# Kernel optimization log

Measured on AMD Instinct MI355X. Metric: run time of the kernel, lower is better.

Reference implementation:

```python
import jax, jax.numpy as jnp
import numpy as np

WS = 8            # window size -> N = 64 tokens per window
DIM = 256
HEADS = 8
BWIN = 4096       # B * num_windows (512x512 image, batch 1)


def _rel_pos_index(ws):
    # exact replica of the torch buffer construction
    coords = np.stack(np.meshgrid(np.arange(ws), np.arange(ws), indexing='ij'))  # (2, ws, ws)
    cf = coords.reshape(2, -1)
    rel = cf[:, :, None] - cf[:, None, :]          # (2, N, N)
    rel = rel.transpose(1, 2, 0).astype(np.int64)  # (N, N, 2)
    rel[..., 0] += ws - 1
    rel[..., 1] += ws - 1
    rel[..., 0] *= 2 * ws - 1
    return np.clip(rel.sum(-1), -1000, 1000)       # (N, N)


def setup_inputs() -> dict:
    key = jax.random.key(0)
    ks = jax.random.split(key, 6)
    N = WS * WS
    x = jax.random.normal(ks[0], (BWIN, N, DIM), dtype=jnp.float32)
    var = jax.random.normal(ks[1], (BWIN, N, DIM), dtype=jnp.float32)
    W_qkv = jax.random.normal(ks[2], (DIM, 3 * DIM), dtype=jnp.float32) * 0.02
    b_qkv = jnp.zeros((3 * DIM,), dtype=jnp.float32)
    W_proj = jax.random.normal(ks[3], (DIM, DIM), dtype=jnp.float32) * 0.02
    b_proj = jnp.zeros((DIM,), dtype=jnp.float32)
    bias_table = jax.random.normal(ks[4], ((2 * WS - 1) * (2 * WS - 1), HEADS), dtype=jnp.float32) * 0.02
    rel_index = jnp.asarray(_rel_pos_index(WS), dtype=jnp.int32)
    return {"x": x, "var": var, "W_qkv": W_qkv, "b_qkv": b_qkv,
            "W_proj": W_proj, "b_proj": b_proj,
            "bias_table": bias_table, "rel_index": rel_index}


def reference(x, var, W_qkv, b_qkv, W_proj, b_proj, bias_table, rel_index):
    B_, N, C = x.shape
    H = HEADS
    hd = C // H
    scale = hd ** -0.5
    topk = int(0.8 * N)  # int(0.8 * ws * ws) = 51

    # --- topk variance modulation mask ---
    var_self = jnp.einsum('bnd,bmd->bnm', var, var)              # (B_, N, N)
    idx = jax.lax.top_k(var_self, topk)[1]                       # (B_, N, topk)
    b_ix = jnp.arange(B_)[:, None, None]
    n_ix = jnp.arange(N)[None, :, None]
    mask = jnp.zeros((B_, N, N), x.dtype).at[b_ix, n_ix, idx].set(1.0)
    mod = jnp.where(mask > 0, jnp.asarray(1.0, x.dtype), jnp.asarray(1.2, x.dtype))
    mod = mod[:, None]                                           # (B_, 1, N, N)

    # --- windowed self-attention with modulation + relative position bias ---
    qkv = (x @ W_qkv + b_qkv).reshape(B_, N, 3, H, hd).transpose(2, 0, 3, 1, 4)
    q, k, v = qkv[0], qkv[1], qkv[2]                             # each (B_, H, N, hd)
    dots = jnp.einsum('bhnd,bhmd->bhnm', q * scale, k) * mod     # (B_, H, N, N)
    bias = bias_table[rel_index.reshape(-1)].reshape(N, N, H).transpose(2, 0, 1)
    dots = dots + bias[None]
    attn = jax.nn.softmax(dots, axis=-1)
    out = jnp.einsum('bhnm,bhmd->bhnd', attn, v)                 # (B_, H, N, hd)
    out = out.transpose(0, 2, 1, 3).reshape(B_, N, C)
    return out @ W_proj + b_proj
```

## Files before the change

### kernel.cpp

```cpp
#include <hip/hip_runtime.h>

#define NTOK 64
#define DIM 256
#define NH 8
#define HD 32
#define BWIN 4096
#define TOPK 51

typedef _Float16 f16;
typedef _Float16 f16x8 __attribute__((ext_vector_type(8)));
typedef _Float16 f16x4 __attribute__((ext_vector_type(4)));
typedef float f32x4 __attribute__((ext_vector_type(4)));

#define MFMA(a, b, c) __builtin_amdgcn_mfma_f32_16x16x32_f16((a), (b), (c), 0, 0, 0)

__global__ void prep_kernel(const float* __restrict__ Wqkv, const float* __restrict__ Wproj,
                            const float* __restrict__ bias_table, const int* __restrict__ rel_index,
                            f16* __restrict__ Wqt, f16* __restrict__ Wpt, float* __restrict__ biasp) {
    int tid = blockIdx.x * blockDim.x + threadIdx.x;
    const int nq = 768 * 256, np = 256 * 256, nb = NH * NTOK * NTOK;
    for (int i = tid; i < nq + np + nb; i += gridDim.x * blockDim.x) {
        if (i < nq) {
            int o = i >> 8, d = i & 255;
            Wqt[i] = (f16)Wqkv[d * 768 + o];
        } else if (i < nq + np) {
            int j = i - nq;
            int o = j >> 8, d = j & 255;
            Wpt[j] = (f16)Wproj[d * 256 + o];
        } else {
            int j = i - nq - np;
            int h = j >> 12;
            int nm = j & 4095;
            biasp[j] = bias_table[rel_index[nm] * NH + h];
        }
    }
}

__global__ __launch_bounds__(256, 2)
void swin_kernel(const float* __restrict__ x, const float* __restrict__ var,
                 const float* __restrict__ b_qkv, const float* __restrict__ b_proj,
                 const f16* __restrict__ Wqt, const f16* __restrict__ Wpt,
                 const float* __restrict__ biasp, float* __restrict__ out) {
    __shared__ __align__(16) union {
        struct {
            f16 xv[64][264];
            union {
                float vs[64][65];
                f16 p[64][72];
            } s2;
            unsigned char mod[64][64];
            f16 qm[64][40];
            f16 km[64][40];
            f16 vT[32][72];
            f16 oh[64][40];
        } a;
        struct {
            f16 pad[64 * 264];
            f16 lo[64][264];
        } b;
    } sm;

    const int tid = threadIdx.x;
    const int lane = tid & 63;
    const int w = tid >> 6;
    const int lc = lane & 15;
    const int lq = lane >> 4;
    const int bwin = blockIdx.x;

    const float* varp = var + (size_t)bwin * NTOK * DIM;
    const float* xp = x + (size_t)bwin * NTOK * DIM;
    float* outp = out + (size_t)bwin * NTOK * DIM;

    #pragma unroll
    for (int it = 0; it < 16; ++it) {
        int i = it * 256 + tid;
        int r = i >> 6, c4 = i & 63;
        float4 v4 = ((const float4*)varp)[i];
        f16 h0 = (f16)v4.x, h1 = (f16)v4.y, h2 = (f16)v4.z, h3 = (f16)v4.w;
        f16x4 hv = {h0, h1, h2, h3};
        f16x4 lv = {(f16)(v4.x - (float)h0), (f16)(v4.y - (float)h1),
                    (f16)(v4.z - (float)h2), (f16)(v4.w - (float)h3)};
        *(f16x4*)&sm.a.xv[r][c4 * 4] = hv;
        *(f16x4*)&sm.b.lo[r][c4 * 4] = lv;
    }
    __syncthreads();

    f32x4 vacc[4];
    #pragma unroll
    for (int mt = 0; mt < 4; ++mt) vacc[mt] = (f32x4){0.f, 0.f, 0.f, 0.f};
    #pragma unroll
    for (int ks = 0; ks < 8; ++ks) {
        int k0 = ks * 32 + lq * 8;
        f16x8 ahi = *(const f16x8*)&sm.a.xv[w * 16 + lc][k0];
        f16x8 alo = *(const f16x8*)&sm.b.lo[w * 16 + lc][k0];
        #pragma unroll
        for (int mt = 0; mt < 4; ++mt) {
            f16x8 bhi = *(const f16x8*)&sm.a.xv[mt * 16 + lc][k0];
            f16x8 blo = *(const f16x8*)&sm.b.lo[mt * 16 + lc][k0];
            vacc[mt] = MFMA(ahi, bhi, vacc[mt]);
            vacc[mt] = MFMA(ahi, blo, vacc[mt]);
            vacc[mt] = MFMA(alo, bhi, vacc[mt]);
        }
    }
    __syncthreads();
    #pragma unroll
    for (int mt = 0; mt < 4; ++mt)
        #pragma unroll
        for (int r = 0; r < 4; ++r)
            sm.a.s2.vs[w * 16 + lq * 4 + r][mt * 16 + lc] = vacc[mt][r];
    __syncthreads();

    float4 xl[16];
    #pragma unroll
    for (int it = 0; it < 16; ++it) xl[it] = ((const float4*)xp)[it * 256 + tid];

    {
        int n = tid >> 2, part = tid & 3;
        float vm[16];
        int cnt[16];
        #pragma unroll
        for (int i = 0; i < 16; ++i) { vm[i] = sm.a.s2.vs[n][part * 16 + i]; cnt[i] = 0; }
        for (int j = 0; j < 64; ++j) {
            float vj = sm.a.s2.vs[n][j];
            #pragma unroll
            for (int i = 0; i < 16; ++i) {
                int mi = part * 16 + i;
                cnt[i] += (int)((vj > vm[i]) | ((vj == vm[i]) & (j < mi)));
            }
        }
        #pragma unroll
        for (int i = 0; i < 16; ++i)
            sm.a.mod[n][part * 16 + i] = (cnt[i] < TOPK) ? 1 : 0;
    }

    #pragma unroll
    for (int it = 0; it < 16; ++it) {
        int i = it * 256 + tid;
        int r = i >> 6, c4 = i & 63;
        float4 v4 = xl[it];
        f16x4 hv = {(f16)v4.x, (f16)v4.y, (f16)v4.z, (f16)v4.w};
        *(f16x4*)&sm.a.xv[r][c4 * 4] = hv;
    }
    __syncthreads();

    f32x4 facc[4][4];
    #pragma unroll
    for (int rt = 0; rt < 4; ++rt)
        #pragma unroll
        for (int pt = 0; pt < 4; ++pt) facc[rt][pt] = (f32x4){0.f, 0.f, 0.f, 0.f};

    const float scale = 0.17677669529663687f;

    for (int h = 0; h < NH; ++h) {
        f32x4 qa[2], ka[2], va[2];
        #pragma unroll
        for (int ct = 0; ct < 2; ++ct) {
            qa[ct] = (f32x4){0.f, 0.f, 0.f, 0.f};
            ka[ct] = (f32x4){0.f, 0.f, 0.f, 0.f};
            va[ct] = (f32x4){0.f, 0.f, 0.f, 0.f};
        }
        #pragma unroll
        for (int ks = 0; ks < 8; ++ks) {
            int k0 = ks * 32 + lq * 8;
            f16x8 af = *(const f16x8*)&sm.a.xv[w * 16 + lc][k0];
            #pragma unroll
            for (int ct = 0; ct < 2; ++ct) {
                int oq = h * 32 + ct * 16 + lc;
                f16x8 bq = *(const f16x8*)&Wqt[(size_t)oq * 256 + k0];
                f16x8 bk = *(const f16x8*)&Wqt[(size_t)(256 + oq) * 256 + k0];
                f16x8 bv = *(const f16x8*)&Wqt[(size_t)(512 + oq) * 256 + k0];
                qa[ct] = MFMA(af, bq, qa[ct]);
                ka[ct] = MFMA(af, bk, ka[ct]);
                va[ct] = MFMA(af, bv, va[ct]);
            }
        }
        #pragma unroll
        for (int ct = 0; ct < 2; ++ct) {
            int oq = h * 32 + ct * 16 + lc;
            float bq = b_qkv[oq], bk = b_qkv[256 + oq], bv = b_qkv[512 + oq];
            #pragma unroll
            for (int r = 0; r < 4; ++r) {
                int row = w * 16 + lq * 4 + r;
                sm.a.qm[row][ct * 16 + lc] = (f16)(qa[ct][r] + bq);
                sm.a.km[row][ct * 16 + lc] = (f16)(ka[ct][r] + bk);
                sm.a.vT[ct * 16 + lc][row] = (f16)(va[ct][r] + bv);
            }
        }
        __syncthreads();

        f32x4 dacc[4];
        {
            f16x8 qf = *(const f16x8*)&sm.a.qm[w * 16 + lc][lq * 8];
            #pragma unroll
            for (int mt = 0; mt < 4; ++mt) {
                f16x8 kf = *(const f16x8*)&sm.a.km[mt * 16 + lc][lq * 8];
                f32x4 zz = {0.f, 0.f, 0.f, 0.f};
                dacc[mt] = MFMA(qf, kf, zz);
            }
        }
        float pv[4][4], mx[4], lsum[4];
        #pragma unroll
        for (int r = 0; r < 4; ++r) mx[r] = -1e30f;
        #pragma unroll
        for (int mt = 0; mt < 4; ++mt)
            #pragma unroll
            for (int r = 0; r < 4; ++r) {
                int row = w * 16 + lq * 4 + r;
                int col = mt * 16 + lc;
                float modv = sm.a.mod[row][col] ? 1.0f : 1.2f;
                float bv = biasp[(h * 64 + row) * 64 + col];
                float t = dacc[mt][r] * scale * modv + bv;
                pv[mt][r] = t;
                mx[r] = fmaxf(mx[r], t);
            }
        #pragma unroll
        for (int r = 0; r < 4; ++r) {
            float m = mx[r];
            m = fmaxf(m, __shfl_xor(m, 1));
            m = fmaxf(m, __shfl_xor(m, 2));
            m = fmaxf(m, __shfl_xor(m, 4));
            m = fmaxf(m, __shfl_xor(m, 8));
            mx[r] = m;
            lsum[r] = 0.f;
        }
        #pragma unroll
        for (int mt = 0; mt < 4; ++mt)
            #pragma unroll
            for (int r = 0; r < 4; ++r) {
                float e = __expf(pv[mt][r] - mx[r]);
                pv[mt][r] = e;
                lsum[r] += e;
            }
        #pragma unroll
        for (int r = 0; r < 4; ++r) {
            float s = lsum[r];
            s += __shfl_xor(s, 1);
            s += __shfl_xor(s, 2);
            s += __shfl_xor(s, 4);
            s += __shfl_xor(s, 8);
            lsum[r] = s;
        }
        #pragma unroll
        for (int mt = 0; mt < 4; ++mt)
            #pragma unroll
            for (int r = 0; r < 4; ++r)
                sm.a.s2.p[w * 16 + lq * 4 + r][mt * 16 + lc] = (f16)pv[mt][r];
        __syncthreads();

        f32x4 oacc[2];
        #pragma unroll
        for (int ct = 0; ct < 2; ++ct) oacc[ct] = (f32x4){0.f, 0.f, 0.f, 0.f};
        #pragma unroll
        for (int ks = 0; ks < 2; ++ks) {
            f16x8 pf = *(const f16x8*)&sm.a.s2.p[w * 16 + lc][ks * 32 + lq * 8];
            #pragma unroll
            for (int ct = 0; ct < 2; ++ct) {
                f16x8 vf = *(const f16x8*)&sm.a.vT[ct * 16 + lc][ks * 32 + lq * 8];
                oacc[ct] = MFMA(pf, vf, oacc[ct]);
            }
        }
        float rl[4];
        #pragma unroll
        for (int r = 0; r < 4; ++r) rl[r] = 1.0f / lsum[r];
        #pragma unroll
        for (int ct = 0; ct < 2; ++ct)
            #pragma unroll
            for (int r = 0; r < 4; ++r)
                sm.a.oh[w * 16 + lq * 4 + r][ct * 16 + lc] = (f16)(oacc[ct][r] * rl[r]);
        __syncthreads();

        #pragma unroll
        for (int rt = 0; rt < 4; ++rt) {
            f16x8 af = *(const f16x8*)&sm.a.oh[rt * 16 + lc][lq * 8];
            #pragma unroll
            for (int pt = 0; pt < 4; ++pt) {
                f16x8 bf = *(const f16x8*)&Wpt[(size_t)(w * 64 + pt * 16 + lc) * 256 + h * 32 + lq * 8];
                facc[rt][pt] = MFMA(af, bf, facc[rt][pt]);
            }
        }
        __syncthreads();
    }

    #pragma unroll
    for (int pt = 0; pt < 4; ++pt) {
        int col = w * 64 + pt * 16 + lc;
        float bp = b_proj[col];
        #pragma unroll
        for (int rt = 0; rt < 4; ++rt)
            #pragma unroll
            for (int r = 0; r < 4; ++r) {
                int row = rt * 16 + lq * 4 + r;
                outp[row * 256 + col] = facc[rt][pt][r] + bp;
            }
    }
}

extern "C" void kernel_launch(void* const* d_in, const int* in_sizes, int n_in,
                              void* d_out, int out_size, void* d_ws, size_t ws_size,
                              hipStream_t stream) {
    const float* x          = (const float*)d_in[0];
    const float* var        = (const float*)d_in[1];
    const float* W_qkv      = (const float*)d_in[2];
    const float* b_qkv      = (const float*)d_in[3];
    const float* W_proj     = (const float*)d_in[4];
    const float* b_proj     = (const float*)d_in[5];
    const float* bias_table = (const float*)d_in[6];
    const int*   rel_index  = (const int*)d_in[7];

    f16*   Wqt   = (f16*)d_ws;
    f16*   Wpt   = (f16*)((char*)d_ws + 393216);
    float* biasp = (float*)((char*)d_ws + 524288);

    prep_kernel<<<288, 256, 0, stream>>>(W_qkv, W_proj, bias_table, rel_index, Wqt, Wpt, biasp);
    swin_kernel<<<BWIN, 256, 0, stream>>>(x, var, b_qkv, b_proj, Wqt, Wpt, biasp, (float*)d_out);
}
```

Measured before the change: 1.418 ms.

## Assign one wave per head with register-resident Q/K/V and 512-thread blocks

Restructures the attention kernel so each of 8 waves owns one head. The waves compute Q, K and V for that head with MFMA and keep them in registers. Scores are computed transposed with 16x16x16 MFMA so the accumulator layout feeds the P·V product directly, which removes the per-head shared-memory round trips and most __syncthreads. The bias table is pre-transposed, the mask is stored transposed, and the projection combines all heads' outputs from shared memory at the end. The trade-offs are more registers per thread and a launch bound of 512 threads with min 4 blocks, which may cause spills or limit occupancy.

```diff
diff --git a/kernel.cpp b/kernel.cpp
--- a/kernel.cpp
+++ b/kernel.cpp
@@ -3,7 +3,6 @@
 #define NTOK 64
 #define DIM 256
 #define NH 8
-#define HD 32
 #define BWIN 4096
 #define TOPK 51
 
@@ -12,7 +11,8 @@
 typedef _Float16 f16x4 __attribute__((ext_vector_type(4)));
 typedef float f32x4 __attribute__((ext_vector_type(4)));
 
-#define MFMA(a, b, c) __builtin_amdgcn_mfma_f32_16x16x32_f16((a), (b), (c), 0, 0, 0)
+#define MFMA32(a, b, c) __builtin_amdgcn_mfma_f32_16x16x32_f16((a), (b), (c), 0, 0, 0)
+#define MFMA16(a, b, c) __builtin_amdgcn_mfma_f32_16x16x16f16((a), (b), (c), 0, 0, 0)
 
 __global__ void prep_kernel(const float* __restrict__ Wqkv, const float* __restrict__ Wproj,
                             const float* __restrict__ bias_table, const int* __restrict__ rel_index,
@@ -31,33 +31,25 @@
             int j = i - nq - np;
             int h = j >> 12;
             int nm = j & 4095;
-            biasp[j] = bias_table[rel_index[nm] * NH + h];
+            int n = nm >> 6, m = nm & 63;
+            biasp[(h << 12) + (m << 6) + n] = bias_table[rel_index[nm] * NH + h];
         }
     }
 }
 
-__global__ __launch_bounds__(256, 2)
+__global__ __launch_bounds__(512, 4)
 void swin_kernel(const float* __restrict__ x, const float* __restrict__ var,
                  const float* __restrict__ b_qkv, const float* __restrict__ b_proj,
                  const f16* __restrict__ Wqt, const f16* __restrict__ Wpt,
                  const float* __restrict__ biasp, float* __restrict__ out) {
-    __shared__ __align__(16) union {
-        struct {
-            f16 xv[64][264];
-            union {
-                float vs[64][65];
-                f16 p[64][72];
-            } s2;
-            unsigned char mod[64][64];
-            f16 qm[64][40];
-            f16 km[64][40];
-            f16 vT[32][72];
-            f16 oh[64][40];
-        } a;
-        struct {
-            f16 pad[64 * 264];
+    __shared__ __align__(16) struct {
+        f16 xv[64][264];
+        union {
+            f16 oh[NH][64][40];
             f16 lo[64][264];
-        } b;
+            float vs[64][65];
+        } u;
+        unsigned char modT[64][65];
     } sm;
 
     const int tid = threadIdx.x;
@@ -71,227 +63,284 @@
     const float* xp = x + (size_t)bwin * NTOK * DIM;
     float* outp = out + (size_t)bwin * NTOK * DIM;
 
-    #pragma unroll
-    for (int it = 0; it < 16; ++it) {
-        int i = it * 256 + tid;
+    float4 v4[8], x4[8];
+    #pragma unroll
+    for (int it = 0; it < 8; ++it) v4[it] = ((const float4*)varp)[it * 512 + tid];
+    #pragma unroll
+    for (int it = 0; it < 8; ++it) x4[it] = ((const float4*)xp)[it * 512 + tid];
+    #pragma unroll
+    for (int it = 0; it < 8; ++it) {
+        int i = it * 512 + tid;
         int r = i >> 6, c4 = i & 63;
-        float4 v4 = ((const float4*)varp)[i];
-        f16 h0 = (f16)v4.x, h1 = (f16)v4.y, h2 = (f16)v4.z, h3 = (f16)v4.w;
+        float4 vv = v4[it];
+        f16 h0 = (f16)vv.x, h1 = (f16)vv.y, h2 = (f16)vv.z, h3 = (f16)vv.w;
         f16x4 hv = {h0, h1, h2, h3};
-        f16x4 lv = {(f16)(v4.x - (float)h0), (f16)(v4.y - (float)h1),
-                    (f16)(v4.z - (float)h2), (f16)(v4.w - (float)h3)};
-        *(f16x4*)&sm.a.xv[r][c4 * 4] = hv;
-        *(f16x4*)&sm.b.lo[r][c4 * 4] = lv;
+        f16x4 lv = {(f16)(vv.x - (float)h0), (f16)(vv.y - (float)h1),
+                    (f16)(vv.z - (float)h2), (f16)(vv.w - (float)h3)};
+        *(f16x4*)&sm.xv[r][c4 * 4] = hv;
+        *(f16x4*)&sm.u.lo[r][c4 * 4] = lv;
     }
     __syncthreads();
 
-    f32x4 vacc[4];
-    #pragma unroll
-    for (int mt = 0; mt < 4; ++mt) vacc[mt] = (f32x4){0.f, 0.f, 0.f, 0.f};
-    #pragma unroll
-    for (int ks = 0; ks < 8; ++ks) {
-        int k0 = ks * 32 + lq * 8;
-        f16x8 ahi = *(const f16x8*)&sm.a.xv[w * 16 + lc][k0];
-        f16x8 alo = *(const f16x8*)&sm.b.lo[w * 16 + lc][k0];
-        #pragma unroll
-        for (int mt = 0; mt < 4; ++mt) {
-            f16x8 bhi = *(const f16x8*)&sm.a.xv[mt * 16 + lc][k0];
-            f16x8 blo = *(const f16x8*)&sm.b.lo[mt * 16 + lc][k0];
-            vacc[mt] = MFMA(ahi, bhi, vacc[mt]);
-            vacc[mt] = MFMA(ahi, blo, vacc[mt]);
-            vacc[mt] = MFMA(alo, bhi, vacc[mt]);
-        }
-    }
-    __syncthreads();
-    #pragma unroll
-    for (int mt = 0; mt < 4; ++mt)
-        #pragma unroll
-        for (int r = 0; r < 4; ++r)
-            sm.a.s2.vs[w * 16 + lq * 4 + r][mt * 16 + lc] = vacc[mt][r];
-    __syncthreads();
-
-    float4 xl[16];
-    #pragma unroll
-    for (int it = 0; it < 16; ++it) xl[it] = ((const float4*)xp)[it * 256 + tid];
-
-    {
-        int n = tid >> 2, part = tid & 3;
-        float vm[16];
-        int cnt[16];
-        #pragma unroll
-        for (int i = 0; i < 16; ++i) { vm[i] = sm.a.s2.vs[n][part * 16 + i]; cnt[i] = 0; }
-        for (int j = 0; j < 64; ++j) {
-            float vj = sm.a.s2.vs[n][j];
-            #pragma unroll
-            for (int i = 0; i < 16; ++i) {
-                int mi = part * 16 + i;
-                cnt[i] += (int)((vj > vm[i]) | ((vj == vm[i]) & (j < mi)));
-            }
-        }
-        #pragma unroll
-        for (int i = 0; i < 16; ++i)
-            sm.a.mod[n][part * 16 + i] = (cnt[i] < TOPK) ? 1 : 0;
-    }
-
-    #pragma unroll
-    for (int it = 0; it < 16; ++it) {
-        int i = it * 256 + tid;
-        int r = i >> 6, c4 = i & 63;
-        float4 v4 = xl[it];
-        f16x4 hv = {(f16)v4.x, (f16)v4.y, (f16)v4.z, (f16)v4.w};
-        *(f16x4*)&sm.a.xv[r][c4 * 4] = hv;
-    }
-    __syncthreads();
-
-    f32x4 facc[4][4];
-    #pragma unroll
-    for (int rt = 0; rt < 4; ++rt)
-        #pragma unroll
-        for (int pt = 0; pt < 4; ++pt) facc[rt][pt] = (f32x4){0.f, 0.f, 0.f, 0.f};
-
-    const float scale = 0.17677669529663687f;
-
-    for (int h = 0; h < NH; ++h) {
-        f32x4 qa[2], ka[2], va[2];
-        #pragma unroll
-        for (int ct = 0; ct < 2; ++ct) {
-            qa[ct] = (f32x4){0.f, 0.f, 0.f, 0.f};
-            ka[ct] = (f32x4){0.f, 0.f, 0.f, 0.f};
-            va[ct] = (f32x4){0.f, 0.f, 0.f, 0.f};
-        }
+    {
+        const int rs = w >> 1;
+        f32x4 vacc[2];
+        vacc[0] = (f32x4){0.f, 0.f, 0.f, 0.f};
+        vacc[1] = (f32x4){0.f, 0.f, 0.f, 0.f};
         #pragma unroll
         for (int ks = 0; ks < 8; ++ks) {
             int k0 = ks * 32 + lq * 8;
-            f16x8 af = *(const f16x8*)&sm.a.xv[w * 16 + lc][k0];
-            #pragma unroll
-            for (int ct = 0; ct < 2; ++ct) {
-                int oq = h * 32 + ct * 16 + lc;
-                f16x8 bq = *(const f16x8*)&Wqt[(size_t)oq * 256 + k0];
-                f16x8 bk = *(const f16x8*)&Wqt[(size_t)(256 + oq) * 256 + k0];
-                f16x8 bv = *(const f16x8*)&Wqt[(size_t)(512 + oq) * 256 + k0];
-                qa[ct] = MFMA(af, bq, qa[ct]);
-                ka[ct] = MFMA(af, bk, ka[ct]);
-                va[ct] = MFMA(af, bv, va[ct]);
-            }
+            f16x8 ahi = *(const f16x8*)&sm.xv[rs * 16 + lc][k0];
+            f16x8 alo = *(const f16x8*)&sm.u.lo[rs * 16 + lc][k0];
+            #pragma unroll
+            for (int m = 0; m < 2; ++m) {
+                int mt = (w & 1) * 2 + m;
+                f16x8 bhi = *(const f16x8*)&sm.xv[mt * 16 + lc][k0];
+                f16x8 blo = *(const f16x8*)&sm.u.lo[mt * 16 + lc][k0];
+                vacc[m] = MFMA32(ahi, bhi, vacc[m]);
+                vacc[m] = MFMA32(ahi, blo, vacc[m]);
+                vacc[m] = MFMA32(alo, bhi, vacc[m]);
+            }
+        }
+        __syncthreads();
+        #pragma unroll
+        for (int m = 0; m < 2; ++m) {
+            int mt = (w & 1) * 2 + m;
+            #pragma unroll
+            for (int r = 0; r < 4; ++r)
+                sm.u.vs[rs * 16 + lq * 4 + r][mt * 16 + lc] = vacc[m][r];
+        }
+    }
+    #pragma unroll
+    for (int it = 0; it < 8; ++it) {
+        int i = it * 512 + tid;
+        int r = i >> 6, c4 = i & 63;
+        float4 vv = x4[it];
+        f16x4 hv = {(f16)vv.x, (f16)vv.y, (f16)vv.z, (f16)vv.w};
+        *(f16x4*)&sm.xv[r][c4 * 4] = hv;
+    }
+    __syncthreads();
+
+    {
+        int n = tid >> 3, part = tid & 7;
+        float vm[8];
+        int cnt[8];
+        #pragma unroll
+        for (int i = 0; i < 8; ++i) { vm[i] = sm.u.vs[n][part * 8 + i]; cnt[i] = 0; }
+        for (int j = 0; j < 64; ++j) {
+            float vj = sm.u.vs[n][j];
+            #pragma unroll
+            for (int i = 0; i < 8; ++i) {
+                int mi = part * 8 + i;
+                cnt[i] += (int)((vj > vm[i]) | ((vj == vm[i]) & (j < mi)));
+            }
+        }
+        #pragma unroll
+        for (int i = 0; i < 8; ++i)
+            sm.modT[part * 8 + i][n] = (cnt[i] < TOPK) ? 1 : 0;
+    }
+    __syncthreads();
+
+    const int h = w;
+    const float scale = 0.17677669529663687f;
+    const f16* Wq = Wqt + (size_t)(h * 32) * 256;
+    const f16* Wk = Wqt + (size_t)(256 + h * 32) * 256;
+    const f16* Wv = Wqt + (size_t)(512 + h * 32) * 256;
+
+    float bqr[2][4], bkr[2][4], bvl[2];
+    #pragma unroll
+    for (int ot = 0; ot < 2; ++ot)
+        #pragma unroll
+        for (int r = 0; r < 4; ++r) {
+            bqr[ot][r] = b_qkv[h * 32 + ot * 16 + lq * 4 + r];
+            bkr[ot][r] = b_qkv[256 + h * 32 + ot * 16 + lq * 4 + r];
+        }
+    #pragma unroll
+    for (int cd = 0; cd < 2; ++cd) bvl[cd] = b_qkv[512 + h * 32 + cd * 16 + lc];
+
+    f16x4 qop[2][4], kop[2][4], vop[2][4];
+    {
+        f32x4 acc[2][4];
+        #pragma unroll
+        for (int a = 0; a < 2; ++a)
+            #pragma unroll
+            for (int b = 0; b < 4; ++b) acc[a][b] = (f32x4){0.f, 0.f, 0.f, 0.f};
+        #pragma unroll
+        for (int ks = 0; ks < 8; ++ks) {
+            int k0 = ks * 32 + lq * 8;
+            f16x8 xf[4], wf[2];
+            #pragma unroll
+            for (int tt = 0; tt < 4; ++tt) xf[tt] = *(const f16x8*)&sm.xv[tt * 16 + lc][k0];
+            #pragma unroll
+            for (int ot = 0; ot < 2; ++ot) wf[ot] = *(const f16x8*)&Wq[(size_t)(ot * 16 + lc) * 256 + k0];
+            #pragma unroll
+            for (int ot = 0; ot < 2; ++ot)
+                #pragma unroll
+                for (int tt = 0; tt < 4; ++tt)
+                    acc[ot][tt] = MFMA32(wf[ot], xf[tt], acc[ot][tt]);
+        }
+        #pragma unroll
+        for (int ot = 0; ot < 2; ++ot)
+            #pragma unroll
+            for (int tt = 0; tt < 4; ++tt)
+                #pragma unroll
+                for (int r = 0; r < 4; ++r)
+                    qop[ot][tt][r] = (f16)((acc[ot][tt][r] + bqr[ot][r]) * scale);
+        #pragma unroll
+        for (int a = 0; a < 2; ++a)
+            #pragma unroll
+            for (int b = 0; b < 4; ++b) acc[a][b] = (f32x4){0.f, 0.f, 0.f, 0.f};
+        #pragma unroll
+        for (int ks = 0; ks < 8; ++ks) {
+            int k0 = ks * 32 + lq * 8;
+            f16x8 xf[4], wf[2];
+            #pragma unroll
+            for (int tt = 0; tt < 4; ++tt) xf[tt] = *(const f16x8*)&sm.xv[tt * 16 + lc][k0];
+            #pragma unroll
+            for (int ot = 0; ot < 2; ++ot) wf[ot] = *(const f16x8*)&Wk[(size_t)(ot * 16 + lc) * 256 + k0];
+            #pragma unroll
+            for (int ot = 0; ot < 2; ++ot)
+                #pragma unroll
+                for (int tt = 0; tt < 4; ++tt)
+                    acc[ot][tt] = MFMA32(wf[ot], xf[tt], acc[ot][tt]);
+        }
+        #pragma unroll
+        for (int ot = 0; ot < 2; ++ot)
+            #pragma unroll
+            for (int tt = 0; tt < 4; ++tt)
+                #pragma unroll
+                for (int r = 0; r < 4; ++r)
+                    kop[ot][tt][r] = (f16)(acc[ot][tt][r] + bkr[ot][r]);
+        #pragma unroll
+        for (int a = 0; a < 2; ++a)
+            #pragma unroll
+            for (int b = 0; b < 4; ++b) acc[a][b] = (f32x4){0.f, 0.f, 0.f, 0.f};
+        #pragma unroll
+        for (int ks = 0; ks < 8; ++ks) {
+            int k0 = ks * 32 + lq * 8;
+            f16x8 xf[4], wf[2];
+            #pragma unroll
+            for (int tt = 0; tt < 4; ++tt) xf[tt] = *(const f16x8*)&sm.xv[tt * 16 + lc][k0];
+            #pragma unroll
+            for (int cd = 0; cd < 2; ++cd) wf[cd] = *(const f16x8*)&Wv[(size_t)(cd * 16 + lc) * 256 + k0];
+            #pragma unroll
+            for (int cd = 0; cd < 2; ++cd)
+                #pragma unroll
+                for (int tt = 0; tt < 4; ++tt)
+                    acc[cd][tt] = MFMA32(xf[tt], wf[cd], acc[cd][tt]);
+        }
+        #pragma unroll
+        for (int cd = 0; cd < 2; ++cd)
+            #pragma unroll
+            for (int tt = 0; tt < 4; ++tt)
+                #pragma unroll
+                for (int r = 0; r < 4; ++r)
+                    vop[cd][tt][r] = (f16)(acc[cd][tt][r] + bvl[cd]);
+    }
+
+    f16x4 pop[4][4];
+    float ls[4];
+    const float* bt = biasp + h * 4096;
+    #pragma unroll
+    for (int ci = 0; ci < 4; ++ci) {
+        f32x4 st[4];
+        #pragma unroll
+        for (int rj = 0; rj < 4; ++rj) {
+            f32x4 z = (f32x4){0.f, 0.f, 0.f, 0.f};
+            z = MFMA16(kop[0][rj], qop[0][ci], z);
+            st[rj] = MFMA16(kop[1][rj], qop[1][ci], z);
+        }
+        float mx = -1e30f;
+        #pragma unroll
+        for (int rj = 0; rj < 4; ++rj)
+            #pragma unroll
+            for (int r = 0; r < 4; ++r) {
+                int j = rj * 16 + lq * 4 + r;
+                float modv = sm.modT[j][ci * 16 + lc] ? 1.0f : 1.2f;
+                float t = st[rj][r] * modv + bt[j * 64 + ci * 16 + lc];
+                st[rj][r] = t;
+                mx = fmaxf(mx, t);
+            }
+        mx = fmaxf(mx, __shfl_xor(mx, 16));
+        mx = fmaxf(mx, __shfl_xor(mx, 32));
+        float s = 0.f;
+        #pragma unroll
+        for (int rj = 0; rj < 4; ++rj)
+            #pragma unroll
+            for (int r = 0; r < 4; ++r) {
+                float e = __expf(st[rj][r] - mx);
+                st[rj][r] = e;
+                s += e;
+            }
+        s += __shfl_xor(s, 16);
+        s += __shfl_xor(s, 32);
+        ls[ci] = s;
+        #pragma unroll
+        for (int rj = 0; rj < 4; ++rj)
+            #pragma unroll
+            for (int r = 0; r < 4; ++r)
+                pop[ci][rj][r] = (f16)st[rj][r];
+    }
+
+    {
+        f32x4 oacc[4][2];
+        #pragma unroll
+        for (int ti = 0; ti < 4; ++ti)
+            #pragma unroll
+            for (int cd = 0; cd < 2; ++cd) oacc[ti][cd] = (f32x4){0.f, 0.f, 0.f, 0.f};
+        #pragma unroll
+        for (int kc = 0; kc < 4; ++kc)
+            #pragma unroll
+            for (int ti = 0; ti < 4; ++ti)
+                #pragma unroll
+                for (int cd = 0; cd < 2; ++cd)
+                    oacc[ti][cd] = MFMA16(pop[ti][kc], vop[cd][kc], oacc[ti][cd]);
+        float inv[4];
+        #pragma unroll
+        for (int ci = 0; ci < 4; ++ci) inv[ci] = 1.0f / ls[ci];
+        #pragma unroll
+        for (int ti = 0; ti < 4; ++ti)
+            #pragma unroll
+            for (int r = 0; r < 4; ++r) {
+                float rl = __shfl(inv[ti], lq * 4 + r);
+                #pragma unroll
+                for (int cd = 0; cd < 2; ++cd)
+                    sm.u.oh[w][ti * 16 + lq * 4 + r][cd * 16 + lc] = (f16)(oacc[ti][cd][r] * rl);
+            }
+    }
+    __syncthreads();
+
+    {
+        f32x4 facc[4][2];
+        #pragma unroll
+        for (int rt = 0; rt < 4; ++rt)
+            #pragma unroll
+            for (int ct = 0; ct < 2; ++ct) facc[rt][ct] = (f32x4){0.f, 0.f, 0.f, 0.f};
+        #pragma unroll
+        for (int hh = 0; hh < NH; ++hh) {
+            f16x8 pf[4], wfp[2];
+            #pragma unroll
+            for (int rt = 0; rt < 4; ++rt)
+                pf[rt] = *(const f16x8*)&sm.u.oh[hh][rt * 16 + lc][lq * 8];
+            #pragma unroll
+            for (int ct = 0; ct < 2; ++ct)
+                wfp[ct] = *(const f16x8*)&Wpt[(size_t)(w * 32 + ct * 16 + lc) * 256 + hh * 32 + lq * 8];
+            #pragma unroll
+            for (int rt = 0; rt < 4; ++rt)
+                #pragma unroll
+                for (int ct = 0; ct < 2; ++ct)
+                    facc[rt][ct] = MFMA32(pf[rt], wfp[ct], facc[rt][ct]);
         }
         #pragma unroll
         for (int ct = 0; ct < 2; ++ct) {
-            int oq = h * 32 + ct * 16 + lc;
-            float bq = b_qkv[oq], bk = b_qkv[256 + oq], bv = b_qkv[512 + oq];
-            #pragma unroll
-            for (int r = 0; r < 4; ++r) {
-                int row = w * 16 + lq * 4 + r;
-                sm.a.qm[row][ct * 16 + lc] = (f16)(qa[ct][r] + bq);
-                sm.a.km[row][ct * 16 + lc] = (f16)(ka[ct][r] + bk);
-                sm.a.vT[ct * 16 + lc][row] = (f16)(va[ct][r] + bv);
-            }
-        }
-        __syncthreads();
-
-        f32x4 dacc[4];
-        {
-            f16x8 qf = *(const f16x8*)&sm.a.qm[w * 16 + lc][lq * 8];
-            #pragma unroll
-            for (int mt = 0; mt < 4; ++mt) {
-                f16x8 kf = *(const f16x8*)&sm.a.km[mt * 16 + lc][lq * 8];
-                f32x4 zz = {0.f, 0.f, 0.f, 0.f};
-                dacc[mt] = MFMA(qf, kf, zz);
-            }
-        }
-        float pv[4][4], mx[4], lsum[4];
-        #pragma unroll
-        for (int r = 0; r < 4; ++r) mx[r] = -1e30f;
-        #pragma unroll
-        for (int mt = 0; mt < 4; ++mt)
-            #pragma unroll
-            for (int r = 0; r < 4; ++r) {
-                int row = w * 16 + lq * 4 + r;
-                int col = mt * 16 + lc;
-                float modv = sm.a.mod[row][col] ? 1.0f : 1.2f;
-                float bv = biasp[(h * 64 + row) * 64 + col];
-                float t = dacc[mt][r] * scale * modv + bv;
-                pv[mt][r] = t;
-                mx[r] = fmaxf(mx[r], t);
-            }
-        #pragma unroll
-        for (int r = 0; r < 4; ++r) {
-            float m = mx[r];
-            m = fmaxf(m, __shfl_xor(m, 1));
-            m = fmaxf(m, __shfl_xor(m, 2));
-            m = fmaxf(m, __shfl_xor(m, 4));
-            m = fmaxf(m, __shfl_xor(m, 8));
-            mx[r] = m;
-            lsum[r] = 0.f;
-        }
-        #pragma unroll
-        for (int mt = 0; mt < 4; ++mt)
-            #pragma unroll
-            for (int r = 0; r < 4; ++r) {
-                float e = __expf(pv[mt][r] - mx[r]);
-                pv[mt][r] = e;
-                lsum[r] += e;
-            }
-        #pragma unroll
-        for (int r = 0; r < 4; ++r) {
-            float s = lsum[r];
-            s += __shfl_xor(s, 1);
-            s += __shfl_xor(s, 2);
-            s += __shfl_xor(s, 4);
-            s += __shfl_xor(s, 8);
-            lsum[r] = s;
-        }
-        #pragma unroll
-        for (int mt = 0; mt < 4; ++mt)
-            #pragma unroll
-            for (int r = 0; r < 4; ++r)
-                sm.a.s2.p[w * 16 + lq * 4 + r][mt * 16 + lc] = (f16)pv[mt][r];
-        __syncthreads();
-
-        f32x4 oacc[2];
-        #pragma unroll
-        for (int ct = 0; ct < 2; ++ct) oacc[ct] = (f32x4){0.f, 0.f, 0.f, 0.f};
-        #pragma unroll
-        for (int ks = 0; ks < 2; ++ks) {
-            f16x8 pf = *(const f16x8*)&sm.a.s2.p[w * 16 + lc][ks * 32 + lq * 8];
-            #pragma unroll
-            for (int ct = 0; ct < 2; ++ct) {
-                f16x8 vf = *(const f16x8*)&sm.a.vT[ct * 16 + lc][ks * 32 + lq * 8];
-                oacc[ct] = MFMA(pf, vf, oacc[ct]);
-            }
-        }
-        float rl[4];
-        #pragma unroll
-        for (int r = 0; r < 4; ++r) rl[r] = 1.0f / lsum[r];
-        #pragma unroll
-        for (int ct = 0; ct < 2; ++ct)
-            #pragma unroll
-            for (int r = 0; r < 4; ++r)
-                sm.a.oh[w * 16 + lq * 4 + r][ct * 16 + lc] = (f16)(oacc[ct][r] * rl[r]);
-        __syncthreads();
-
-        #pragma unroll
-        for (int rt = 0; rt < 4; ++rt) {
-            f16x8 af = *(const f16x8*)&sm.a.oh[rt * 16 + lc][lq * 8];
-            #pragma unroll
-            for (int pt = 0; pt < 4; ++pt) {
-                f16x8 bf = *(const f16x8*)&Wpt[(size_t)(w * 64 + pt * 16 + lc) * 256 + h * 32 + lq * 8];
-                facc[rt][pt] = MFMA(af, bf, facc[rt][pt]);
-            }
-        }
-        __syncthreads();
-    }
-
-    #pragma unroll
-    for (int pt = 0; pt < 4; ++pt) {
-        int col = w * 64 + pt * 16 + lc;
-        float bp = b_proj[col];
-        #pragma unroll
-        for (int rt = 0; rt < 4; ++rt)
-            #pragma unroll
-            for (int r = 0; r < 4; ++r) {
-                int row = rt * 16 + lq * 4 + r;
-                outp[row * 256 + col] = facc[rt][pt][r] + bp;
-            }
+            int col = w * 32 + ct * 16 + lc;
+            float bp = b_proj[col];
+            #pragma unroll
+            for (int rt = 0; rt < 4; ++rt)
+                #pragma unroll
+                for (int r = 0; r < 4; ++r)
+                    outp[(rt * 16 + lq * 4 + r) * 256 + col] = facc[rt][ct][r] + bp;
+        }
     }
 }
 
@@ -312,5 +361,5 @@
     float* biasp = (float*)((char*)d_ws + 524288);
 
     prep_kernel<<<288, 256, 0, stream>>>(W_qkv, W_proj, bias_table, rel_index, Wqt, Wpt, biasp);
-    swin_kernel<<<BWIN, 256, 0, stream>>>(x, var, b_qkv, b_proj, Wqt, Wpt, biasp, (float*)d_out);
+    swin_kernel<<<BWIN, 512, 0, stream>>>(x, var, b_qkv, b_proj, Wqt, Wpt, biasp, (float*)d_out);
 }
```

After: 1.398 ms. No clear change (-1.4%).
